# Optimization experiments

Measured on AMD Instinct MI355X. Metric: run time of the kernel, lower is better.

Reference implementation:

```python
import jax, jax.numpy as jnp
import numpy as np

D_MODEL = 1024
NUM_HEADS = 16
WINDOW = 2048  # must equal seq_len (see notes): source matmul attn(B,H,S,W) @ v(B,H,S,hd) requires W == S
SEQ_LEN = 2048
BATCH = 1


def setup_inputs() -> dict:
    key = jax.random.key(0)
    k0, k1, k2 = jax.random.split(key, 3)
    d = D_MODEL
    x = jax.random.normal(k0, (BATCH, SEQ_LEN, d), dtype=jnp.float32)
    w_qkv = jax.random.normal(k1, (3 * d, d), dtype=jnp.float32) * (d ** -0.5)
    b_qkv = jnp.zeros((3 * d,), dtype=jnp.float32)
    w_proj = jax.random.normal(k2, (d, d), dtype=jnp.float32) * (d ** -0.5)
    b_proj = jnp.zeros((d,), dtype=jnp.float32)
    return {"x": x, "w_qkv": w_qkv, "b_qkv": b_qkv, "w_proj": w_proj, "b_proj": b_proj}


def reference(x, w_qkv, b_qkv, w_proj, b_proj):
    B, S, d = x.shape
    H = NUM_HEADS
    hd = d // H
    W = WINDOW
    scale = hd ** -0.5

    # qkv projection (torch Linear: x @ W^T + b)
    qkv = x @ w_qkv.T + b_qkv                      # (B, S, 3d)
    qkv = qkv.reshape(B, S, 3, H, hd).transpose(2, 0, 3, 1, 4)  # (3, B, H, S, hd)
    q, k, v = qkv[0], qkv[1], qkv[2]

    # sliding-window scores: score[b,h,i,j] = q_i . k_padded[i+j] * scale, j in [0, W)
    pad = W // 2
    k_pad = jnp.pad(k, ((0, 0), (0, 0), (pad, pad), (0, 0)))     # (B, H, S+W, hd)
    scores_full = jnp.einsum('bhid,bhjd->bhij', q, k_pad) * scale  # (B, H, S, S+W)
    idx = jnp.arange(S)[:, None] + jnp.arange(W)[None, :]          # (S, W) banded gather indices
    scores = jnp.take_along_axis(scores_full, idx[None, None], axis=-1)  # (B, H, S, W)

    attn = jax.nn.softmax(scores, axis=-1)
    attn = jnp.nan_to_num(attn)  # faithful to torch.nan_to_num(attn, 0.0)

    # Faithful to the source: forward() does matmul(attn, v), i.e. column j of the
    # windowed attn indexes v position j directly (requires W == S).
    out = jnp.einsum('bhij,bhjd->bhid', attn, v)   # (B, H, S, hd)
    out = out.transpose(0, 2, 1, 3).reshape(B, S, d)
    out = out @ w_proj.T + b_proj
    return out, attn
```

## Files before the change

kernel.cpp:

```cpp
#include <hip/hip_runtime.h>
#include <hip/hip_bf16.h>

typedef __hip_bfloat16 bf16;
typedef __attribute__((ext_vector_type(8))) short short8;
typedef __attribute__((ext_vector_type(4))) float f32x4;
typedef __attribute__((ext_vector_type(4))) unsigned short ushort4v;

#define DEV static __device__ __forceinline__

static constexpr int SEQ = 2048;
static constexpr int DM  = 1024;
static constexpr int NH  = 16;
static constexpr int HD  = 64;
static constexpr int WIN = 2048;
static constexpr int PAD = 1024;

DEV void async16(const void* g, void* l) {
  __builtin_amdgcn_global_load_lds(
      (__attribute__((address_space(1))) void*)(g),
      (__attribute__((address_space(3))) void*)(l), 16, 0, 0);
}

__global__ __launch_bounds__(256) void k_cvt(const float* __restrict__ x,
                                             const float* __restrict__ wq,
                                             const float* __restrict__ wp,
                                             bf16* __restrict__ xb,
                                             bf16* __restrict__ wqb,
                                             bf16* __restrict__ wpb) {
  const int NX = SEQ * DM, NQ = 3 * DM * DM, NP = DM * DM;
  const int tot = (NX + NQ + NP) >> 2;
  const int stride = gridDim.x * 256;
  for (int i = blockIdx.x * 256 + threadIdx.x; i < tot; i += stride) {
    int e = i << 2;
    const float* s; bf16* d; int o;
    if (e < NX)            { s = x;  d = xb;  o = e; }
    else if (e < NX + NQ)  { s = wq; d = wqb; o = e - NX; }
    else                   { s = wp; d = wpb; o = e - NX - NQ; }
    float4 v = *(const float4*)(s + o);
    __align__(8) bf16 t4[4] = {__float2bfloat16(v.x), __float2bfloat16(v.y),
                               __float2bfloat16(v.z), __float2bfloat16(v.w)};
    *(uint2*)(d + o) = *(uint2*)t4;
  }
}

DEV void gemm_core(const bf16* __restrict__ A, const bf16* __restrict__ B,
                   int m0, int n0, int K, int tid, bf16* As, bf16* Bs,
                   f32x4 (&acc)[4][4]) {
  const int lane = tid & 63, wid = tid >> 6;
  const int wm = wid >> 1, wn = wid & 1;
  const int l15 = lane & 15, l4 = lane >> 4;
  for (int k0 = 0; k0 < K; k0 += 64) {
    __syncthreads();
    #pragma unroll
    for (int it = 0; it < 4; ++it) {
      int rb = it * 32 + wid * 8;
      int r  = rb + (lane >> 3);
      int c  = (lane & 7) * 8;
      async16(A + (size_t)(m0 + r) * K + k0 + c, As + rb * 64);
      async16(B + (size_t)(n0 + r) * K + k0 + c, Bs + rb * 64);
    }
    asm volatile("s_waitcnt vmcnt(0)" ::: "memory");
    __syncthreads();
    #pragma unroll
    for (int kk = 0; kk < 2; ++kk) {
      short8 a[4], b[4];
      #pragma unroll
      for (int im = 0; im < 4; ++im)
        a[im] = *(const short8*)(As + (wm * 64 + im * 16 + l15) * 64 + kk * 32 + l4 * 8);
      #pragma unroll
      for (int in = 0; in < 4; ++in)
        b[in] = *(const short8*)(Bs + (wn * 64 + in * 16 + l15) * 64 + kk * 32 + l4 * 8);
      #pragma unroll
      for (int im = 0; im < 4; ++im)
        #pragma unroll
        for (int in = 0; in < 4; ++in)
          acc[im][in] = __builtin_amdgcn_mfma_f32_16x16x32_bf16(a[im], b[in], acc[im][in], 0, 0, 0);
    }
  }
}

__global__ __launch_bounds__(256) void k_gemm_qkv(const bf16* __restrict__ A,
                                                  const bf16* __restrict__ B,
                                                  const float* __restrict__ bias,
                                                  bf16* __restrict__ qo,
                                                  bf16* __restrict__ ko,
                                                  bf16* __restrict__ vt) {
  __shared__ bf16 As[128 * 64], Bs[128 * 64];
  const int tid = threadIdx.x, lane = tid & 63;
  const int wid = tid >> 6, wm = wid >> 1, wn = wid & 1;
  const int l15 = lane & 15, l4 = lane >> 4;
  const int m0 = blockIdx.x * 128, n0 = blockIdx.y * 128;
  f32x4 acc[4][4] = {};
  gemm_core(A, B, m0, n0, DM, tid, As, Bs, acc);
  #pragma unroll
  for (int im = 0; im < 4; ++im)
    #pragma unroll
    for (int in = 0; in < 4; ++in) {
      int col = n0 + wn * 64 + in * 16 + l15;
      float bval = bias[col];
      int t = col >> 10, h = (col >> 6) & 15, dd = col & 63;
      int row0 = m0 + wm * 64 + im * 16 + l4 * 4;
      if (t == 2) {
        __align__(8) bf16 t4[4];
        #pragma unroll
        for (int r = 0; r < 4; ++r)
          t4[r] = __float2bfloat16(acc[im][in][r] + bval);
        *(uint2*)&vt[((size_t)h * HD + dd) * SEQ + row0] = *(uint2*)t4;
      } else {
        #pragma unroll
        for (int r = 0; r < 4; ++r) {
          float v = acc[im][in][r] + bval;
          size_t idx = ((size_t)h * SEQ + row0 + r) * HD + dd;
          if (t == 0) qo[idx] = __float2bfloat16(v * 0.18033688011112042f);
          else        ko[idx] = __float2bfloat16(v);
        }
      }
    }
}

DEV void stage_kp(const bf16* kbase, int i0, int tt, int lane, bf16* dst) {
  #pragma unroll
  for (int it = 0; it < 4; ++it) {
    int r  = it * 8 + (lane >> 3);
    int cg = lane & 7;
    int jp = i0 + tt * 32 + r;
    int krow = jp - PAD;
    krow = krow < 0 ? 0 : (krow > SEQ - 1 ? SEQ - 1 : krow);
    int sc = (cg ^ (r & 7)) * 8;
    async16(kbase + (size_t)krow * HD + sc, dst + it * 8 * 64);
  }
}

DEV void qk_mfma_lds(const bf16* KPb, const short8 (&qf)[2][2], int l15, int l4,
                     f32x4 (&sf)[2][2]) {
  __builtin_amdgcn_s_setprio(1);
  #pragma unroll
  for (int kg = 0; kg < 2; ++kg) {
    short8 kfr[2];
    #pragma unroll
    for (int fn = 0; fn < 2; ++fn) {
      int jl = fn * 16 + l15;
      int pg = (kg * 4 + l4) ^ (jl & 7);
      kfr[fn] = *(const short8*)&KPb[jl * 64 + pg * 8];
    }
    #pragma unroll
    for (int fm = 0; fm < 2; ++fm)
      #pragma unroll
      for (int fn = 0; fn < 2; ++fn)
        sf[fm][fn] = __builtin_amdgcn_mfma_f32_16x16x32_bf16(qf[fm][kg], kfr[fn], sf[fm][fn], 0, 0, 0);
  }
  __builtin_amdgcn_s_setprio(0);
}

DEV void qk_mfma_lds_sw(const bf16* KPb, const short8 (&qf)[2][2], int l15, int l4,
                        f32x4 (&sf)[2][2]) {
  __builtin_amdgcn_s_setprio(1);
  #pragma unroll
  for (int kg = 0; kg < 2; ++kg) {
    short8 kfr[2];
    #pragma unroll
    for (int fj = 0; fj < 2; ++fj) {
      int jl = fj * 16 + l15;
      int pg = (kg * 4 + l4) ^ (jl & 7);
      kfr[fj] = *(const short8*)&KPb[jl * 64 + pg * 8];
    }
    #pragma unroll
    for (int fj = 0; fj < 2; ++fj)
      #pragma unroll
      for (int fi = 0; fi < 2; ++fi)
        sf[fj][fi] = __builtin_amdgcn_mfma_f32_16x16x32_bf16(kfr[fj], qf[fi][kg], sf[fj][fi], 0, 0, 0);
  }
  __builtin_amdgcn_s_setprio(0);
}

DEV int pad_lo(int i0) { int d = PAD - i0; return d <= 0 ? 0 : (d >> 5); }
DEV int pad_hi(int i0) { int t = ((PAD + SEQ - 1 - i0) >> 5) + 1; return t > 65 ? 65 : t; }

__global__ __launch_bounds__(256) void k_attn(const bf16* __restrict__ q,
                                              const bf16* __restrict__ kkk,
                                              const bf16* __restrict__ vT,
                                              float* __restrict__ attn,
                                              bf16* __restrict__ ao) {
  const int h  = blockIdx.x >> 6;
  const int i0 = (blockIdx.x & 63) << 5;
  const int tid = threadIdx.x;
  const int c = tid >> 6;
  const int lane = tid & 63;
  const int l15 = lane & 15, l4 = lane >> 4;
  const int lo_g = pad_lo(i0), hi_g = pad_hi(i0);

  __shared__ bf16 KP[4][2][32 * 64];
  __shared__ unsigned short JFB[4][32 * 64];
  __shared__ float sums[4][32];
  __shared__ float invL[32];

  short8 qf[2][2];
  #pragma unroll
  for (int fm = 0; fm < 2; ++fm)
    #pragma unroll
    for (int kg = 0; kg < 2; ++kg)
      qf[fm][kg] = *(const short8*)&q[((size_t)h * SEQ + i0 + fm * 16 + l15) * HD + kg * 32 + l4 * 8];

  const bf16* kbase = kkk + (size_t)h * SEQ * HD;
  const bf16* vbase = vT + (size_t)h * HD * SEQ;
  float* abase = attn + (size_t)(h * SEQ + i0) * WIN;

  {
    constexpr int st[5] = {0, 16, 32, 48, 65};
    int lo = st[c] > lo_g ? st[c] : lo_g;
    int hi = st[c + 1] < hi_g ? st[c + 1] : hi_g;

    float psum[2] = {0.f, 0.f};
    if (lo < hi) {
      stage_kp(kbase, i0, lo, lane, KP[c][lo & 1]);
      for (int tt = lo; tt < hi; ++tt) {
        int nxt = (tt + 1 < hi) ? tt + 1 : tt;
        stage_kp(kbase, i0, nxt, lane, KP[c][(tt + 1) & 1]);
        asm volatile("s_waitcnt vmcnt(4)" ::: "memory");
        f32x4 sf[2][2] = {};
        qk_mfma_lds_sw(KP[c][tt & 1], qf, l15, l4, sf);
        const bool interior = (tt >= 1) && (tt <= 63) &&
                              (i0 + tt * 32 >= PAD) && (i0 + tt * 32 + 31 < PAD + SEQ);
        if (interior) {
          #pragma unroll
          for (int fj = 0; fj < 2; ++fj)
            #pragma unroll
            for (int r = 0; r < 4; ++r) {
              psum[0] += __builtin_amdgcn_exp2f(sf[fj][0][r]);
              psum[1] += __builtin_amdgcn_exp2f(sf[fj][1][r]);
            }
        } else {
          #pragma unroll
          for (int fj = 0; fj < 2; ++fj)
            #pragma unroll
            for (int r = 0; r < 4; ++r) {
              int jj = tt * 32 + fj * 16 + l4 * 4 + r;
              int jp = i0 + jj;
              bool pad = (jp < PAD) || (jp >= PAD + SEQ);
              #pragma unroll
              for (int fi = 0; fi < 2; ++fi) {
                int iloc = fi * 16 + l15;
                float e = pad ? 1.0f : __builtin_amdgcn_exp2f(sf[fj][fi][r]);
                if ((unsigned)(jj - iloc) < (unsigned)WIN) psum[fi] += e;
              }
            }
        }
      }
    }
    float r0 = psum[0];
    r0 += __shfl_xor(r0, 16); r0 += __shfl_xor(r0, 32);
    float r1 = psum[1];
    r1 += __shfl_xor(r1, 16); r1 += __shfl_xor(r1, 32);
    if (lane < 32) {
      int i_abs = i0 + lane;
      float s = (lane < 16) ? r0 : r1;
      if (c == 0) {
        int cl = i0 + lo_g * 32 - i_abs; if (cl < 0) cl = 0;
        int cr = i_abs + WIN - (i0 + hi_g * 32); if (cr < 0) cr = 0;
        s += (float)(cl + cr);
      }
      sums[c][lane] = s;
    }
  }
  __syncthreads();
  if (tid < 32)
    invL[tid] = __builtin_amdgcn_rcpf(sums[0][tid] + sums[1][tid] +
                                      sums[2][tid] + sums[3][tid]);
  __syncthreads();

  float invf[4];
  #pragma unroll
  for (int s2 = 0; s2 < 4; ++s2) invf[s2] = invL[s2 * 8 + (lane >> 3)];

  const int c0 = c * 16, c1 = c0 + 16;
  unsigned short* JW = JFB[c];
  f32x4 oacc[2][4] = {};
  stage_kp(kbase, i0, c0, lane, KP[c][0]);
  for (int tt = c0; tt <= c1; ++tt) {
    short8 bv[4];
    if (tt > c0) {
      int jb = (tt - 1) * 32;
      #pragma unroll
      for (int nd = 0; nd < 4; ++nd)
        bv[nd] = *(const short8*)&vbase[(size_t)(nd * 16 + l15) * SEQ + jb + l4 * 8];
    }
    int nxt = (tt < c1) ? tt + 1 : tt;
    stage_kp(kbase, i0, nxt, lane, KP[c][(tt + 1) & 1]);
    if (tt == c0)          asm volatile("s_waitcnt vmcnt(4)" ::: "memory");
    else if (tt == c0 + 1) asm volatile("s_waitcnt vmcnt(8)" ::: "memory");
    else                   asm volatile("s_waitcnt vmcnt(12)" ::: "memory");

    const bool fp = (tt < lo_g) || (tt >= hi_g);
    f32x4 sf[2][2] = {};
    if (!fp) qk_mfma_lds(KP[c][tt & 1], qf, l15, l4, sf);

    const bool allv = (i0 + tt * 32 >= PAD) && (i0 + tt * 32 + 31 < PAD + SEQ);
    #pragma unroll
    for (int fm = 0; fm < 2; ++fm)
      #pragma unroll
      for (int fn = 0; fn < 2; ++fn) {
        int J0 = tt * 32 + fn * 16 + l15;
        bool padc = fp || (!allv && ((i0 + J0 < PAD) || (i0 + J0 >= PAD + SEQ)));
        #pragma unroll
        for (int r = 0; r < 4; ++r) {
          int row = fm * 16 + l4 * 4 + r;
          float e = padc ? 1.0f : __builtin_amdgcn_exp2f(sf[fm][fn][r]);
          int j6 = (J0 - row) & 63;
          int sg = (j6 >> 3) ^ (row & 7);
          JW[row * 64 + sg * 8 + (j6 & 7)] = __bfloat16_as_ushort(__float2bfloat16(e));
        }
      }

    if (tt > c0) {
      const int g = (tt - 1) & 1;
      const int Jb = (tt - 1) * 32;
      const int c8 = lane & 7;
      #pragma unroll
      for (int s2 = 0; s2 < 4; ++s2) {
        int row = s2 * 8 + (lane >> 3);
        int sg = (g * 4 + (c8 >> 1)) ^ (row & 7);
        ushort4v uv = *(const ushort4v*)&JW[row * 64 + sg * 8 + (c8 & 1) * 4];
        f32x4 vv;
        #pragma unroll
        for (int e = 0; e < 4; ++e)
          vv[e] = __uint_as_float((unsigned)uv[e] << 16) * invf[s2];
        __builtin_nontemporal_store(vv, (f32x4*)(abase + (size_t)row * WIN + Jb + c8 * 4));
      }
      short8 af[2];
      #pragma unroll
      for (int fm = 0; fm < 2; ++fm) {
        int row = fm * 16 + l15;
        int sg = (g * 4 + l4) ^ (row & 7);
        af[fm] = *(const short8*)&JW[row * 64 + sg * 8];
      }
      __builtin_amdgcn_s_setprio(1);
      #pragma unroll
      for (int fm = 0; fm < 2; ++fm)
        #pragma unroll
        for (int nd = 0; nd < 4; ++nd)
          oacc[fm][nd] = __builtin_amdgcn_mfma_f32_16x16x32_bf16(af[fm], bv[nd], oacc[fm][nd], 0, 0, 0);
      __builtin_amdgcn_s_setprio(0);
    }
  }

  __syncthreads();
  float* OX = (float*)&KP[0][0][0];
  float* OW = OX + c * 2048;
  #pragma unroll
  for (int fm = 0; fm < 2; ++fm)
    #pragma unroll
    for (int nd = 0; nd < 4; ++nd)
      #pragma unroll
      for (int r = 0; r < 4; ++r)
        OW[(fm * 16 + l4 * 4 + r) * 64 + nd * 16 + l15] = oacc[fm][nd][r];
  __syncthreads();
  {
    int row = tid >> 3;
    int d0 = (tid & 7) * 8;
    float iv = invL[row];
    union { unsigned short u[8]; short8 v; } o;
    #pragma unroll
    for (int e = 0; e < 8; ++e) {
      int idx = row * 64 + d0 + e;
      float s = (OX[idx] + OX[2048 + idx] + OX[4096 + idx] + OX[6144 + idx]) * iv;
      o.u[e] = __bfloat16_as_ushort(__float2bfloat16(s));
    }
    *(short8*)&ao[(size_t)(i0 + row) * DM + h * HD + d0] = o.v;
  }
}

__global__ __launch_bounds__(256) void k_gemm_proj(const bf16* __restrict__ A,
                                                   const bf16* __restrict__ B,
                                                   const float* __restrict__ bias,
                                                   float* __restrict__ out) {
  __shared__ bf16 As[128 * 64], Bs[128 * 64];
  const int tid = threadIdx.x, lane = tid & 63;
  const int wid = tid >> 6, wm = wid >> 1, wn = wid & 1;
  const int l15 = lane & 15, l4 = lane >> 4;
  const int m0 = blockIdx.x * 128, n0 = blockIdx.y * 128;
  f32x4 acc[4][4] = {};
  gemm_core(A, B, m0, n0, DM, tid, As, Bs, acc);
  #pragma unroll
  for (int im = 0; im < 4; ++im)
    #pragma unroll
    for (int in = 0; in < 4; ++in) {
      int col = n0 + wn * 64 + in * 16 + l15;
      float bval = bias[col];
      #pragma unroll
      for (int r = 0; r < 4; ++r) {
        int row = m0 + wm * 64 + im * 16 + l4 * 4 + r;
        out[(size_t)row * DM + col] = acc[im][in][r] + bval;
      }
    }
}

extern "C" void kernel_launch(void* const* d_in, const int* in_sizes, int n_in,
                              void* d_out, int out_size, void* d_ws, size_t ws_size,
                              hipStream_t stream) {
  (void)in_sizes; (void)n_in; (void)out_size; (void)ws_size;
  const float* x  = (const float*)d_in[0];
  const float* wq = (const float*)d_in[1];
  const float* bq = (const float*)d_in[2];
  const float* wp = (const float*)d_in[3];
  const float* bp = (const float*)d_in[4];
  float* out  = (float*)d_out;
  float* attn = out + (size_t)SEQ * DM;

  char* ws = (char*)d_ws;
  bf16* xb    = (bf16*)(ws + (size_t) 0);
  bf16* wqb   = (bf16*)(ws + ((size_t)4  << 20));
  bf16* wpb   = (bf16*)(ws + ((size_t)10 << 20));
  bf16* qarr  = (bf16*)(ws + ((size_t)12 << 20));
  bf16* karr  = (bf16*)(ws + ((size_t)16 << 20));
  bf16* vt    = (bf16*)(ws + ((size_t)24 << 20));
  bf16* ao    = (bf16*)(ws + ((size_t)28 << 20));

  k_cvt<<<dim3(1024), dim3(256), 0, stream>>>(x, wq, wp, xb, wqb, wpb);
  k_gemm_qkv<<<dim3(16, 24), dim3(256), 0, stream>>>(xb, wqb, bq, qarr, karr, vt);
  k_attn<<<dim3(1024), dim3(256), 0, stream>>>(qarr, karr, vt, attn, ao);
  k_gemm_proj<<<dim3(16, 8), dim3(256), 0, stream>>>(ao, wpb, bp, out);
}
```

Before: 150.5 us.

## Shrink GEMM M-tile to 64, remap attention blocks across XCDs, use cached attn stores

Both GEMMs now use 64x128 tiles instead of 128x128, which doubles the grid (768 and 256 blocks) so the 256 CUs are filled better, especially for the small projection GEMM. The attention kernel remaps block IDs so that consecutive blocks of a head land on the same XCD, improving L2 reuse of K/V. The probability stores switch from nontemporal to regular stores. The smaller tiles cost more global traffic per FLOP, and regular stores may pollute the cache with the large attn output.

```diff
diff --git a/kernel.cpp b/kernel.cpp
--- a/kernel.cpp
+++ b/kernel.cpp
@@ -43,37 +43,42 @@
   }
 }
 
-DEV void gemm_core(const bf16* __restrict__ A, const bf16* __restrict__ B,
-                   int m0, int n0, int K, int tid, bf16* As, bf16* Bs,
-                   f32x4 (&acc)[4][4]) {
+DEV void gemm_core64(const bf16* __restrict__ A, const bf16* __restrict__ B,
+                     int m0, int n0, int K, int tid, bf16* As, bf16* Bs,
+                     f32x4 (&acc)[4][2]) {
   const int lane = tid & 63, wid = tid >> 6;
-  const int wm = wid >> 1, wn = wid & 1;
   const int l15 = lane & 15, l4 = lane >> 4;
   for (int k0 = 0; k0 < K; k0 += 64) {
     __syncthreads();
+    #pragma unroll
+    for (int it = 0; it < 2; ++it) {
+      int rb = it * 32 + wid * 8;
+      int r  = rb + (lane >> 3);
+      int c  = (lane & 7) * 8;
+      async16(A + (size_t)(m0 + r) * K + k0 + c, As + rb * 64);
+    }
     #pragma unroll
     for (int it = 0; it < 4; ++it) {
       int rb = it * 32 + wid * 8;
       int r  = rb + (lane >> 3);
       int c  = (lane & 7) * 8;
-      async16(A + (size_t)(m0 + r) * K + k0 + c, As + rb * 64);
       async16(B + (size_t)(n0 + r) * K + k0 + c, Bs + rb * 64);
     }
     asm volatile("s_waitcnt vmcnt(0)" ::: "memory");
     __syncthreads();
     #pragma unroll
     for (int kk = 0; kk < 2; ++kk) {
-      short8 a[4], b[4];
+      short8 a[4], b[2];
       #pragma unroll
       for (int im = 0; im < 4; ++im)
-        a[im] = *(const short8*)(As + (wm * 64 + im * 16 + l15) * 64 + kk * 32 + l4 * 8);
-      #pragma unroll
-      for (int in = 0; in < 4; ++in)
-        b[in] = *(const short8*)(Bs + (wn * 64 + in * 16 + l15) * 64 + kk * 32 + l4 * 8);
+        a[im] = *(const short8*)(As + (im * 16 + l15) * 64 + kk * 32 + l4 * 8);
+      #pragma unroll
+      for (int in = 0; in < 2; ++in)
+        b[in] = *(const short8*)(Bs + (wid * 32 + in * 16 + l15) * 64 + kk * 32 + l4 * 8);
       #pragma unroll
       for (int im = 0; im < 4; ++im)
         #pragma unroll
-        for (int in = 0; in < 4; ++in)
+        for (int in = 0; in < 2; ++in)
           acc[im][in] = __builtin_amdgcn_mfma_f32_16x16x32_bf16(a[im], b[in], acc[im][in], 0, 0, 0);
     }
   }
@@ -85,21 +90,21 @@
                                                   bf16* __restrict__ qo,
                                                   bf16* __restrict__ ko,
                                                   bf16* __restrict__ vt) {
-  __shared__ bf16 As[128 * 64], Bs[128 * 64];
+  __shared__ bf16 As[64 * 64], Bs[128 * 64];
   const int tid = threadIdx.x, lane = tid & 63;
-  const int wid = tid >> 6, wm = wid >> 1, wn = wid & 1;
+  const int wid = tid >> 6;
   const int l15 = lane & 15, l4 = lane >> 4;
-  const int m0 = blockIdx.x * 128, n0 = blockIdx.y * 128;
-  f32x4 acc[4][4] = {};
-  gemm_core(A, B, m0, n0, DM, tid, As, Bs, acc);
+  const int m0 = blockIdx.x * 64, n0 = blockIdx.y * 128;
+  f32x4 acc[4][2] = {};
+  gemm_core64(A, B, m0, n0, DM, tid, As, Bs, acc);
   #pragma unroll
   for (int im = 0; im < 4; ++im)
     #pragma unroll
-    for (int in = 0; in < 4; ++in) {
-      int col = n0 + wn * 64 + in * 16 + l15;
+    for (int in = 0; in < 2; ++in) {
+      int col = n0 + wid * 32 + in * 16 + l15;
       float bval = bias[col];
       int t = col >> 10, h = (col >> 6) & 15, dd = col & 63;
-      int row0 = m0 + wm * 64 + im * 16 + l4 * 4;
+      int row0 = m0 + im * 16 + l4 * 4;
       if (t == 2) {
         __align__(8) bf16 t4[4];
         #pragma unroll
@@ -181,8 +186,9 @@
                                               const bf16* __restrict__ vT,
                                               float* __restrict__ attn,
                                               bf16* __restrict__ ao) {
-  const int h  = blockIdx.x >> 6;
-  const int i0 = (blockIdx.x & 63) << 5;
+  const int wgid = (blockIdx.x & 7) * 128 + (blockIdx.x >> 3);
+  const int h  = wgid >> 6;
+  const int i0 = (wgid & 63) << 5;
   const int tid = threadIdx.x;
   const int c = tid >> 6;
   const int lane = tid & 63;
@@ -324,7 +330,7 @@
         #pragma unroll
         for (int e = 0; e < 4; ++e)
           vv[e] = __uint_as_float((unsigned)uv[e] << 16) * invf[s2];
-        __builtin_nontemporal_store(vv, (f32x4*)(abase + (size_t)row * WIN + Jb + c8 * 4));
+        *(f32x4*)(abase + (size_t)row * WIN + Jb + c8 * 4) = vv;
       }
       short8 af[2];
       #pragma unroll
@@ -373,22 +379,22 @@
                                                    const bf16* __restrict__ B,
                                                    const float* __restrict__ bias,
                                                    float* __restrict__ out) {
-  __shared__ bf16 As[128 * 64], Bs[128 * 64];
+  __shared__ bf16 As[64 * 64], Bs[128 * 64];
   const int tid = threadIdx.x, lane = tid & 63;
-  const int wid = tid >> 6, wm = wid >> 1, wn = wid & 1;
+  const int wid = tid >> 6;
   const int l15 = lane & 15, l4 = lane >> 4;
-  const int m0 = blockIdx.x * 128, n0 = blockIdx.y * 128;
-  f32x4 acc[4][4] = {};
-  gemm_core(A, B, m0, n0, DM, tid, As, Bs, acc);
+  const int m0 = blockIdx.x * 64, n0 = blockIdx.y * 128;
+  f32x4 acc[4][2] = {};
+  gemm_core64(A, B, m0, n0, DM, tid, As, Bs, acc);
   #pragma unroll
   for (int im = 0; im < 4; ++im)
     #pragma unroll
-    for (int in = 0; in < 4; ++in) {
-      int col = n0 + wn * 64 + in * 16 + l15;
+    for (int in = 0; in < 2; ++in) {
+      int col = n0 + wid * 32 + in * 16 + l15;
       float bval = bias[col];
       #pragma unroll
       for (int r = 0; r < 4; ++r) {
-        int row = m0 + wm * 64 + im * 16 + l4 * 4 + r;
+        int row = m0 + im * 16 + l4 * 4 + r;
         out[(size_t)row * DM + col] = acc[im][in][r] + bval;
       }
     }
@@ -416,7 +422,7 @@
   bf16* ao    = (bf16*)(ws + ((size_t)28 << 20));
 
   k_cvt<<<dim3(1024), dim3(256), 0, stream>>>(x, wq, wp, xb, wqb, wpb);
-  k_gemm_qkv<<<dim3(16, 24), dim3(256), 0, stream>>>(xb, wqb, bq, qarr, karr, vt);
+  k_gemm_qkv<<<dim3(32, 24), dim3(256), 0, stream>>>(xb, wqb, bq, qarr, karr, vt);
   k_attn<<<dim3(1024), dim3(256), 0, stream>>>(qarr, karr, vt, attn, ao);
-  k_gemm_proj<<<dim3(16, 8), dim3(256), 0, stream>>>(ao, wpb, bp, out);
-}
+  k_gemm_proj<<<dim3(32, 8), dim3(256), 0, stream>>>(ao, wpb, bp, out);
+}
```

After: 145.8 us. 3.1% less time.
